# Optimization experiments

Measured on AMD Instinct MI355X. Metric: run time of the kernel, lower is better.

Reference implementation:

```python
import jax, jax.numpy as jnp
import numpy as np

TAU = 0.07
EPS = 1e-6  # torch CosineSimilarity eps


def setup_inputs() -> dict:
    key = jax.random.key(0)
    k1, k2, k3 = jax.random.split(key, 3)
    n, d, n_classes = 8192, 256, 1024
    imitation_embeds = jax.random.normal(k1, (n, d), dtype=jnp.float32)
    recording_embeds = jax.random.normal(k2, (n, d), dtype=jnp.float32)
    labels = jax.random.randint(k3, (n,), 0, n_classes, dtype=jnp.int64)
    return {
        "imitation_embeds": imitation_embeds,
        "recording_embeds": recording_embeds,
        "labels": labels,
    }


def reference(imitation_embeds, recording_embeds, labels):
    n = imitation_embeds.shape[0]
    # cosine similarity with per-vector norm clamp (torch semantics)
    im_n = imitation_embeds / jnp.maximum(
        jnp.linalg.norm(imitation_embeds, axis=1, keepdims=True), EPS)
    rec_n = recording_embeds / jnp.maximum(
        jnp.linalg.norm(recording_embeds, axis=1, keepdims=True), EPS)
    i2r = jnp.einsum("nd,md->nm", im_n, rec_n) / TAU  # [n, n]

    same = labels[:, None] == labels[None, :]          # [n, n] bool
    eye = jnp.eye(n, dtype=bool)
    # original: mask = ~(same ^ diag_embed(diag(same))); diag(same) is all True
    # -> keep the diagonal (positive) and all different-label negatives
    mask = ~(same ^ eye)

    # per-row masked log-softmax evaluated at the diagonal entry:
    # log_softmax(row[mask])[pos_of_diag] = i2r[i,i] - logsumexp(row over mask)
    lse = jax.nn.logsumexp(jnp.where(mask, i2r, -jnp.inf), axis=1)  # [n]
    loss = -jnp.mean(jnp.diagonal(i2r) - lse)
    return loss
```

## Files before the change

### kernel.cpp

```cpp
#include <hip/hip_runtime.h>

#define N 8192
#define D 256
#define INV_TAU 14.285714285714286f
#define EPSN 1e-6f

#define RT 128
#define CT 64
#define CSPLIT 16
#define CPB (N / CSPLIT)
#define NTILES (CPB / CT)
#define LDSS 264

typedef unsigned int u32x4 __attribute__((ext_vector_type(4)));
typedef __bf16 bf16x8 __attribute__((ext_vector_type(8)));
typedef float f32x4 __attribute__((ext_vector_type(4)));

__device__ inline unsigned short f2bf(float x) {
    unsigned int u = __builtin_bit_cast(unsigned int, x);
    u += 0x7fffu + ((u >> 16) & 1u);
    return (unsigned short)(u >> 16);
}

__global__ void ntx_prep(const float* __restrict__ im, const float* __restrict__ rec,
                         unsigned short* __restrict__ A, unsigned short* __restrict__ Bm,
                         float* __restrict__ diag, float* __restrict__ rowsum) {
    const int wave = threadIdx.x >> 6;
    const int lane = threadIdx.x & 63;
    const int row  = blockIdx.x * 4 + wave;

    const float4 a = ((const float4*)(im  + (size_t)row * D))[lane];
    const float4 b = ((const float4*)(rec + (size_t)row * D))[lane];

    float ssa = a.x*a.x + a.y*a.y + a.z*a.z + a.w*a.w;
    float ssb = b.x*b.x + b.y*b.y + b.z*b.z + b.w*b.w;
    float dt  = a.x*b.x + a.y*b.y + a.z*b.z + a.w*b.w;
    #pragma unroll
    for (int o = 32; o; o >>= 1) {
        ssa += __shfl_xor(ssa, o);
        ssb += __shfl_xor(ssb, o);
        dt  += __shfl_xor(dt , o);
    }
    const float ra = 1.0f / fmaxf(sqrtf(ssa), EPSN);
    const float rb = 1.0f / fmaxf(sqrtf(ssb), EPSN);

    ushort4 pa, pb;
    pa.x = f2bf(a.x*ra); pa.y = f2bf(a.y*ra); pa.z = f2bf(a.z*ra); pa.w = f2bf(a.w*ra);
    pb.x = f2bf(b.x*rb); pb.y = f2bf(b.y*rb); pb.z = f2bf(b.z*rb); pb.w = f2bf(b.w*rb);
    *(ushort4*)(A  + (size_t)row * D + lane * 4) = pa;
    *(ushort4*)(Bm + (size_t)row * D + lane * 4) = pb;

    if (lane == 0) {
        diag[row]   = dt * ra * rb * INV_TAU;
        rowsum[row] = 0.0f;
    }
}

__global__ __launch_bounds__(256, 2)
void ntx_lse(const unsigned short* __restrict__ A, const unsigned short* __restrict__ Bm,
             const int* __restrict__ labels, float* __restrict__ rowsum) {
    __shared__ __align__(16) unsigned short Bs[CT][LDSS];

    const int wave = threadIdx.x >> 6;
    const int lane = threadIdx.x & 63;
    const int g    = lane >> 4;
    const int n16  = lane & 15;

    const int rowblk = blockIdx.x & (N / RT - 1);
    const int colblk = blockIdx.x >> 6;
    const int row0 = rowblk * RT + wave * 32;
    const int col0 = colblk * CPB;

    bf16x8 afrag[2][8];
    #pragma unroll
    for (int rs = 0; rs < 2; ++rs) {
        const int r = row0 + rs * 16 + n16;
        #pragma unroll
        for (int k = 0; k < 8; ++k)
            afrag[rs][k] = __builtin_bit_cast(
                bf16x8, *(const u32x4*)(A + (size_t)r * D + k * 32 + g * 8));
    }

    int rlab[2][4];
    #pragma unroll
    for (int rs = 0; rs < 2; ++rs)
        #pragma unroll
        for (int q = 0; q < 4; ++q)
            rlab[rs][q] = labels[row0 + rs * 16 + g * 4 + q];

    float acc[2][4] = {{0.f,0.f,0.f,0.f},{0.f,0.f,0.f,0.f}};

    const int c32 = threadIdx.x & 31;
    const int rr  = threadIdx.x >> 5;

    for (int t = 0; t < NTILES; ++t) {
        const int colt = col0 + t * CT;
        #pragma unroll
        for (int p = 0; p < 8; ++p) {
            const int br = p * 8 + rr;
            u32x4 v = *(const u32x4*)(Bm + (size_t)(colt + br) * D + c32 * 8);
            *(u32x4*)(&Bs[br][c32 * 8]) = v;
        }
        __syncthreads();

        #pragma unroll
        for (int cs = 0; cs < 4; ++cs) {
            const int bc = cs * 16 + n16;
            bf16x8 bfrag[8];
            #pragma unroll
            for (int k = 0; k < 8; ++k)
                bfrag[k] = __builtin_bit_cast(
                    bf16x8, *(const u32x4*)(&Bs[bc][k * 32 + g * 8]));

            const int col  = colt + cs * 16 + n16;
            const int clab = labels[col];

            #pragma unroll
            for (int rs = 0; rs < 2; ++rs) {
                f32x4 c = {0.f, 0.f, 0.f, 0.f};
                #pragma unroll
                for (int k = 0; k < 8; ++k)
                    c = __builtin_amdgcn_mfma_f32_16x16x32_bf16(
                            afrag[rs][k], bfrag[k], c, 0, 0, 0);
                #pragma unroll
                for (int q = 0; q < 4; ++q) {
                    const int r = row0 + rs * 16 + g * 4 + q;
                    const float e = __expf(c[q] * INV_TAU);
                    const bool drop = (rlab[rs][q] == clab) && (r != col);
                    acc[rs][q] += drop ? 0.0f : e;
                }
            }
        }
        __syncthreads();
    }

    #pragma unroll
    for (int rs = 0; rs < 2; ++rs)
        #pragma unroll
        for (int q = 0; q < 4; ++q) {
            float v = acc[rs][q];
            v += __shfl_xor(v, 1);
            v += __shfl_xor(v, 2);
            v += __shfl_xor(v, 4);
            v += __shfl_xor(v, 8);
            if (n16 == 0)
                atomicAdd(&rowsum[row0 + rs * 16 + g * 4 + q], v);
        }
}

__global__ void ntx_finish(const float* __restrict__ diag,
                           const float* __restrict__ rowsum,
                           float* __restrict__ out) {
    __shared__ float red[256];
    float s = 0.f;
    for (int i = threadIdx.x; i < N; i += 256)
        s += logf(rowsum[i]) - diag[i];
    red[threadIdx.x] = s;
    __syncthreads();
    #pragma unroll
    for (int o = 128; o; o >>= 1) {
        if (threadIdx.x < o) red[threadIdx.x] += red[threadIdx.x + o];
        __syncthreads();
    }
    if (threadIdx.x == 0) out[0] = red[0] / (float)N;
}

extern "C" void kernel_launch(void* const* d_in, const int* in_sizes, int n_in,
                              void* d_out, int out_size, void* d_ws, size_t ws_size,
                              hipStream_t stream) {
    const float* im     = (const float*)d_in[0];
    const float* rec    = (const float*)d_in[1];
    const int*   labels = (const int*)d_in[2];
    float* out = (float*)d_out;

    unsigned short* A  = (unsigned short*)d_ws;
    unsigned short* Bm = A + (size_t)N * D;
    float* diag   = (float*)(Bm + (size_t)N * D);
    float* rowsum = diag + N;

    ntx_prep<<<N / 4, 256, 0, stream>>>(im, rec, A, Bm, diag, rowsum);
    ntx_lse<<<(N / RT) * CSPLIT, 256, 0, stream>>>(A, Bm, labels, rowsum);
    ntx_finish<<<1, 256, 0, stream>>>(diag, rowsum, out);
}
```

Baseline: 125.6 us.

## Subtract same-label terms in sparse correction pass instead of masking in GEMM loop

The main GEMM+exp kernel now sums exp over all columns without label masking, and folds 1/tau into the bf16 A operand so the per-element scale multiply is also gone. A new finish kernel finds same-label off-diagonal pairs by ballot over the labels, recomputes their dot products from the bf16 operands, and subtracts their exps from the row sum before the log. The B tile loads are register-prefetched one tile ahead to overlap global loads with MFMA work. The subtraction of a nearly-equal sum risks cancellation error, and the correction kernel scans all labels for each row.

```diff
diff --git a/kernel.cpp b/kernel.cpp
--- a/kernel.cpp
+++ b/kernel.cpp
@@ -22,9 +22,14 @@
     return (unsigned short)(u >> 16);
 }
 
+__device__ inline float bf2f(unsigned short u) {
+    return __builtin_bit_cast(float, (unsigned int)u << 16);
+}
+
 __global__ void ntx_prep(const float* __restrict__ im, const float* __restrict__ rec,
                          unsigned short* __restrict__ A, unsigned short* __restrict__ Bm,
-                         float* __restrict__ diag, float* __restrict__ rowsum) {
+                         float* __restrict__ diag, float* __restrict__ rowsum,
+                         float* __restrict__ out) {
     const int wave = threadIdx.x >> 6;
     const int lane = threadIdx.x & 63;
     const int row  = blockIdx.x * 4 + wave;
@@ -43,9 +48,10 @@
     }
     const float ra = 1.0f / fmaxf(sqrtf(ssa), EPSN);
     const float rb = 1.0f / fmaxf(sqrtf(ssb), EPSN);
+    const float sa = ra * INV_TAU;
 
     ushort4 pa, pb;
-    pa.x = f2bf(a.x*ra); pa.y = f2bf(a.y*ra); pa.z = f2bf(a.z*ra); pa.w = f2bf(a.w*ra);
+    pa.x = f2bf(a.x*sa); pa.y = f2bf(a.y*sa); pa.z = f2bf(a.z*sa); pa.w = f2bf(a.w*sa);
     pb.x = f2bf(b.x*rb); pb.y = f2bf(b.y*rb); pb.z = f2bf(b.z*rb); pb.w = f2bf(b.w*rb);
     *(ushort4*)(A  + (size_t)row * D + lane * 4) = pa;
     *(ushort4*)(Bm + (size_t)row * D + lane * 4) = pb;
@@ -54,11 +60,12 @@
         diag[row]   = dt * ra * rb * INV_TAU;
         rowsum[row] = 0.0f;
     }
+    if (blockIdx.x == 0 && threadIdx.x == 0) out[0] = 0.0f;
 }
 
 __global__ __launch_bounds__(256, 2)
 void ntx_lse(const unsigned short* __restrict__ A, const unsigned short* __restrict__ Bm,
-             const int* __restrict__ labels, float* __restrict__ rowsum) {
+             float* __restrict__ rowsum) {
     __shared__ __align__(16) unsigned short Bs[CT][LDSS];
 
     const int wave = threadIdx.x >> 6;
@@ -81,27 +88,28 @@
                 bf16x8, *(const u32x4*)(A + (size_t)r * D + k * 32 + g * 8));
     }
 
-    int rlab[2][4];
-    #pragma unroll
-    for (int rs = 0; rs < 2; ++rs)
-        #pragma unroll
-        for (int q = 0; q < 4; ++q)
-            rlab[rs][q] = labels[row0 + rs * 16 + g * 4 + q];
-
     float acc[2][4] = {{0.f,0.f,0.f,0.f},{0.f,0.f,0.f,0.f}};
 
     const int c32 = threadIdx.x & 31;
     const int rr  = threadIdx.x >> 5;
 
+    u32x4 stg[8];
+    #pragma unroll
+    for (int p = 0; p < 8; ++p)
+        stg[p] = *(const u32x4*)(Bm + (size_t)(col0 + p * 8 + rr) * D + c32 * 8);
+
     for (int t = 0; t < NTILES; ++t) {
-        const int colt = col0 + t * CT;
-        #pragma unroll
-        for (int p = 0; p < 8; ++p) {
-            const int br = p * 8 + rr;
-            u32x4 v = *(const u32x4*)(Bm + (size_t)(colt + br) * D + c32 * 8);
-            *(u32x4*)(&Bs[br][c32 * 8]) = v;
-        }
+        #pragma unroll
+        for (int p = 0; p < 8; ++p)
+            *(u32x4*)(&Bs[p * 8 + rr][c32 * 8]) = stg[p];
         __syncthreads();
+
+        if (t + 1 < NTILES) {
+            const int coln = col0 + (t + 1) * CT;
+            #pragma unroll
+            for (int p = 0; p < 8; ++p)
+                stg[p] = *(const u32x4*)(Bm + (size_t)(coln + p * 8 + rr) * D + c32 * 8);
+        }
 
         #pragma unroll
         for (int cs = 0; cs < 4; ++cs) {
@@ -111,9 +119,6 @@
             for (int k = 0; k < 8; ++k)
                 bfrag[k] = __builtin_bit_cast(
                     bf16x8, *(const u32x4*)(&Bs[bc][k * 32 + g * 8]));
-
-            const int col  = colt + cs * 16 + n16;
-            const int clab = labels[col];
 
             #pragma unroll
             for (int rs = 0; rs < 2; ++rs) {
@@ -123,12 +128,8 @@
                     c = __builtin_amdgcn_mfma_f32_16x16x32_bf16(
                             afrag[rs][k], bfrag[k], c, 0, 0, 0);
                 #pragma unroll
-                for (int q = 0; q < 4; ++q) {
-                    const int r = row0 + rs * 16 + g * 4 + q;
-                    const float e = __expf(c[q] * INV_TAU);
-                    const bool drop = (rlab[rs][q] == clab) && (r != col);
-                    acc[rs][q] += drop ? 0.0f : e;
-                }
+                for (int q = 0; q < 4; ++q)
+                    acc[rs][q] += __expf(c[q]);
             }
         }
         __syncthreads();
@@ -148,21 +149,62 @@
         }
 }
 
-__global__ void ntx_finish(const float* __restrict__ diag,
-                           const float* __restrict__ rowsum,
-                           float* __restrict__ out) {
-    __shared__ float red[256];
-    float s = 0.f;
-    for (int i = threadIdx.x; i < N; i += 256)
-        s += logf(rowsum[i]) - diag[i];
-    red[threadIdx.x] = s;
+__global__ void ntx_cfin(const unsigned short* __restrict__ A,
+                         const unsigned short* __restrict__ Bm,
+                         const int* __restrict__ labels,
+                         const float* __restrict__ diag,
+                         const float* __restrict__ rowsum,
+                         float* __restrict__ out) {
+    __shared__ float red[4];
+    const int wave = threadIdx.x >> 6;
+    const int lane = threadIdx.x & 63;
+    const int r0 = blockIdx.x * 16 + wave * 4;
+
+    int lab[4];
+    float af[4][4];
+    #pragma unroll
+    for (int r = 0; r < 4; ++r) {
+        lab[r] = labels[r0 + r];
+        const ushort4 av = *(const ushort4*)(A + (size_t)(r0 + r) * D + lane * 4);
+        af[r][0] = bf2f(av.x); af[r][1] = bf2f(av.y);
+        af[r][2] = bf2f(av.z); af[r][3] = bf2f(av.w);
+    }
+    float corr[4] = {0.f, 0.f, 0.f, 0.f};
+
+    for (int it = 0; it < N / 256; ++it) {
+        const int4 lv = ((const int4*)labels)[it * 64 + lane];
+        #pragma unroll
+        for (int s = 0; s < 4; ++s) {
+            const int jl = (s == 0) ? lv.x : (s == 1) ? lv.y : (s == 2) ? lv.z : lv.w;
+            #pragma unroll
+            for (int r = 0; r < 4; ++r) {
+                unsigned long long bm = __ballot(jl == lab[r]);
+                while (bm) {
+                    const int b = __ffsll((unsigned long long)bm) - 1;
+                    bm &= bm - 1;
+                    const int j = (it * 64 + b) * 4 + s;
+                    if (j == r0 + r) continue;
+                    const ushort4 bv = *(const ushort4*)(Bm + (size_t)j * D + lane * 4);
+                    float d = af[r][0]*bf2f(bv.x) + af[r][1]*bf2f(bv.y)
+                            + af[r][2]*bf2f(bv.z) + af[r][3]*bf2f(bv.w);
+                    #pragma unroll
+                    for (int o = 32; o; o >>= 1) d += __shfl_xor(d, o);
+                    corr[r] += __expf(d);
+                }
+            }
+        }
+    }
+
+    if (lane == 0) {
+        float s = 0.f;
+        #pragma unroll
+        for (int r = 0; r < 4; ++r)
+            s += logf(rowsum[r0 + r] - corr[r]) - diag[r0 + r];
+        red[wave] = s;
+    }
     __syncthreads();
-    #pragma unroll
-    for (int o = 128; o; o >>= 1) {
-        if (threadIdx.x < o) red[threadIdx.x] += red[threadIdx.x + o];
-        __syncthreads();
-    }
-    if (threadIdx.x == 0) out[0] = red[0] / (float)N;
+    if (threadIdx.x == 0)
+        atomicAdd(out, (red[0] + red[1] + red[2] + red[3]) * (1.0f / (float)N));
 }
 
 extern "C" void kernel_launch(void* const* d_in, const int* in_sizes, int n_in,
@@ -178,7 +220,7 @@
     float* diag   = (float*)(Bm + (size_t)N * D);
     float* rowsum = diag + N;
 
-    ntx_prep<<<N / 4, 256, 0, stream>>>(im, rec, A, Bm, diag, rowsum);
-    ntx_lse<<<(N / RT) * CSPLIT, 256, 0, stream>>>(A, Bm, labels, rowsum);
-    ntx_finish<<<1, 256, 0, stream>>>(diag, rowsum, out);
-}
+    ntx_prep<<<N / 4, 256, 0, stream>>>(im, rec, A, Bm, diag, rowsum, out);
+    ntx_lse<<<(N / RT) * CSPLIT, 256, 0, stream>>>(A, Bm, rowsum);
+    ntx_cfin<<<N / 16, 256, 0, stream>>>(A, Bm, labels, diag, rowsum, out);
+}
```

Measured after the change: 143.5 us. +14.2%, slower.
